# Kernel optimization log

Hardware: AMD Instinct MI355X
Metric: run time of the kernel (lower is better)

The kernel has to match this reference:

```python
import jax, jax.numpy as jnp
import numpy as np

IGNORE_INDEX = -100
LSE_SQUARE_SCALE = 1e-4  # z_loss coefficient


def setup_inputs() -> dict:
    key = jax.random.key(0)
    k1, k2, k3, k4 = jax.random.split(key, 4)
    N, D, V = 4096, 2048, 50257
    inp = {
        "input": jax.random.normal(k1, (N, D), dtype=jnp.float32),
        "weight": jax.random.normal(k2, (V, D), dtype=jnp.float32) * (D ** -0.5),
        "bias": jnp.zeros((V,), dtype=jnp.float32),
        "target": jax.random.randint(k3, (N,), 0, V, dtype=jnp.int64),
    }
    return inp


def reference(input, weight, bias, target):
    # logits: [N, V] = input @ weight.T + bias  (the GEMM the fused kernel chunks)
    logits = jnp.einsum("nd,vd->nv", input, weight) + bias
    lse = jax.nn.logsumexp(logits, axis=-1)  # [N]
    valid = target != IGNORE_INDEX
    safe_tgt = jnp.where(valid, target, 0)
    tgt_logit = jnp.take_along_axis(logits, safe_tgt[:, None], axis=-1)[:, 0]
    ce = lse - tgt_logit                      # per-token cross entropy
    z = LSE_SQUARE_SCALE * lse * lse          # per-token z-loss (lse_square_scale * lse^2)
    per_token = jnp.where(valid, ce + z, 0.0)
    n_valid = jnp.maximum(jnp.sum(valid), 1).astype(per_token.dtype)
    loss = jnp.sum(per_token) / n_valid       # mean over non-ignored tokens (includes z-loss)
    z_loss = jnp.sum(jnp.where(valid, z, 0.0)) / n_valid
    return loss, z_loss
```

## Files before the change

### kernel.cpp

```cpp
#include <hip/hip_runtime.h>
#include <hip/hip_bf16.h>
#include <stdint.h>

#define N_TOK 4096
#define DIM   2048
#define VOCAB 50257
#define VPAD  50304
#define IGNORE_IDX (-100)

typedef short  bf16x8 __attribute__((ext_vector_type(8)));
typedef float  f32x4  __attribute__((ext_vector_type(4)));
typedef unsigned short u16x8 __attribute__((ext_vector_type(8)));

typedef const __attribute__((address_space(1))) unsigned int* gptr_t;
typedef __attribute__((address_space(3))) unsigned int*       lptr_t;

__device__ __forceinline__ unsigned short f2bf(float f) {
  union { float f; uint32_t u; } c; c.f = f;
  uint32_t u = c.u;
  return (unsigned short)((u + 0x7FFFu + ((u >> 16) & 1u)) >> 16);
}

__global__ void cvt_weight(const float* __restrict__ w, unsigned short* __restrict__ o) {
  const int t   = blockIdx.x * 256 + threadIdx.x;
  const int idx = t << 3;
  const int v   = idx >> 11;
  u16x8 r = {0, 0, 0, 0, 0, 0, 0, 0};
  if (v < VOCAB) {
    const float4* p = (const float4*)(w + idx);
    const float4 x0 = p[0];
    const float4 x1 = p[1];
    r[0] = f2bf(x0.x); r[1] = f2bf(x0.y); r[2] = f2bf(x0.z); r[3] = f2bf(x0.w);
    r[4] = f2bf(x1.x); r[5] = f2bf(x1.y); r[6] = f2bf(x1.z); r[7] = f2bf(x1.w);
  }
  *(u16x8*)(o + idx) = r;
}

__global__ void cvt_input(const float* __restrict__ a, unsigned short* __restrict__ o) {
  const int t   = blockIdx.x * 256 + threadIdx.x;
  const int idx = t << 3;
  const float4* p = (const float4*)(a + idx);
  const float4 x0 = p[0];
  const float4 x1 = p[1];
  u16x8 r;
  r[0] = f2bf(x0.x); r[1] = f2bf(x0.y); r[2] = f2bf(x0.z); r[3] = f2bf(x0.w);
  r[4] = f2bf(x1.x); r[5] = f2bf(x1.y); r[6] = f2bf(x1.z); r[7] = f2bf(x1.w);
  *(u16x8*)(o + idx) = r;
}

__global__ __launch_bounds__(256) void flce_gemm(
    const unsigned short* __restrict__ A,
    const unsigned short* __restrict__ B,
    const float* __restrict__ bias,
    const int* __restrict__ target,
    float* __restrict__ sumexp,
    float* __restrict__ tgtlog)
{
  __shared__ unsigned short As[128 * 32];
  __shared__ unsigned short Bs[128 * 32];
  __shared__ int tgt_s[128];

  const int tid  = threadIdx.x;
  const int lane = tid & 63;
  const int wave = tid >> 6;
  const int wm   = wave >> 1;
  const int wn   = wave & 1;
  const int m0   = blockIdx.x * 128;
  const int v0   = blockIdx.y * 128;

  if (tid < 128) tgt_s[tid] = target[m0 + tid];

  const int r0 = tid >> 2;
  const int c0 = (tid & 3) * 8;
  const unsigned short* ag0 = A + (m0 + r0)      * DIM + c0;
  const unsigned short* ag1 = A + (m0 + 64 + r0) * DIM + c0;
  const unsigned short* bg0 = B + (v0 + r0)      * DIM + c0;
  const unsigned short* bg1 = B + (v0 + 64 + r0) * DIM + c0;
  unsigned short* al0 = As + tid * 8;
  unsigned short* al1 = As + (tid + 256) * 8;
  unsigned short* bl0 = Bs + tid * 8;
  unsigned short* bl1 = Bs + (tid + 256) * 8;

  f32x4 acc[4][4];
#pragma unroll
  for (int i = 0; i < 4; i++)
#pragma unroll
    for (int j = 0; j < 4; j++) acc[i][j] = (f32x4){0.f, 0.f, 0.f, 0.f};

  const int mrow = lane & 15;
  const int quad = lane >> 4;

  for (int kt = 0; kt < DIM; kt += 32) {
    __syncthreads();
    __builtin_amdgcn_global_load_lds((gptr_t)(const void*)(ag0 + kt), (lptr_t)(void*)al0, 16, 0, 0);
    __builtin_amdgcn_global_load_lds((gptr_t)(const void*)(ag1 + kt), (lptr_t)(void*)al1, 16, 0, 0);
    __builtin_amdgcn_global_load_lds((gptr_t)(const void*)(bg0 + kt), (lptr_t)(void*)bl0, 16, 0, 0);
    __builtin_amdgcn_global_load_lds((gptr_t)(const void*)(bg1 + kt), (lptr_t)(void*)bl1, 16, 0, 0);
    __syncthreads();

    bf16x8 av[4], bv[4];
#pragma unroll
    for (int f = 0; f < 4; f++)
      av[f] = *(const bf16x8*)(As + (wm * 64 + f * 16 + mrow) * 32 + quad * 8);
#pragma unroll
    for (int f = 0; f < 4; f++)
      bv[f] = *(const bf16x8*)(Bs + (wn * 64 + f * 16 + mrow) * 32 + quad * 8);

#pragma unroll
    for (int i = 0; i < 4; i++)
#pragma unroll
      for (int j = 0; j < 4; j++)
        acc[i][j] = __builtin_amdgcn_mfma_f32_16x16x32_bf16(av[i], bv[j], acc[i][j], 0, 0, 0);
  }

  const int colb = v0 + wn * 64;
#pragma unroll
  for (int i = 0; i < 4; i++) {
    const int rowl = wm * 64 + i * 16 + quad * 4;
    float rs[4] = {0.f, 0.f, 0.f, 0.f};
#pragma unroll
    for (int j = 0; j < 4; j++) {
      const int colg = colb + j * 16 + mrow;
      if (colg < VOCAB) {
        const float bvv = bias[colg];
#pragma unroll
        for (int r = 0; r < 4; r++) {
          const float lg = acc[i][j][r] + bvv;
          rs[r] += __expf(lg);
          if (tgt_s[rowl + r] == colg) tgtlog[m0 + rowl + r] = lg;
        }
      }
    }
#pragma unroll
    for (int r = 0; r < 4; r++) {
      float v = rs[r];
      v += __shfl_xor(v, 1);
      v += __shfl_xor(v, 2);
      v += __shfl_xor(v, 4);
      v += __shfl_xor(v, 8);
      if (mrow == 0) atomicAdd(&sumexp[m0 + rowl + r], v);
    }
  }
}

__global__ void flce_final(const float* __restrict__ sumexp,
                           const float* __restrict__ tgtlog,
                           const int* __restrict__ target,
                           float* __restrict__ out) {
  const int tid = threadIdx.x;
  float ls = 0.f, zs = 0.f;
  int cnt = 0;
  for (int r = tid; r < N_TOK; r += 256) {
    const int t = target[r];
    if (t != IGNORE_IDX) {
      const float lse = logf(sumexp[r]);
      const float z = 1e-4f * lse * lse;
      ls += (lse - tgtlog[r]) + z;
      zs += z;
      cnt++;
    }
  }
#pragma unroll
  for (int off = 32; off > 0; off >>= 1) {
    ls += __shfl_down(ls, off);
    zs += __shfl_down(zs, off);
    cnt += __shfl_down(cnt, off);
  }
  __shared__ float sls[4], szs[4];
  __shared__ int scnt[4];
  const int lane = tid & 63, wv = tid >> 6;
  if (lane == 0) { sls[wv] = ls; szs[wv] = zs; scnt[wv] = cnt; }
  __syncthreads();
  if (tid == 0) {
    float L = 0.f, Z = 0.f;
    int C = 0;
    for (int w = 0; w < 4; w++) { L += sls[w]; Z += szs[w]; C += scnt[w]; }
    const float n = (float)(C > 0 ? C : 1);
    out[0] = L / n;
    out[1] = Z / n;
  }
}

extern "C" void kernel_launch(void* const* d_in, const int* in_sizes, int n_in,
                              void* d_out, int out_size, void* d_ws, size_t ws_size,
                              hipStream_t stream) {
  const float* input  = (const float*)d_in[0];
  const float* weight = (const float*)d_in[1];
  const float* bias   = (const float*)d_in[2];
  const int*   target = (const int*)d_in[3];
  float* out = (float*)d_out;

  unsigned short* wbf = (unsigned short*)d_ws;
  unsigned short* abf = wbf + (size_t)VPAD * DIM;
  float* sumexp = (float*)(abf + (size_t)N_TOK * DIM);
  float* tgtlog = sumexp + N_TOK;

  hipMemsetAsync(sumexp, 0, N_TOK * sizeof(float), stream);
  cvt_weight<<<(VPAD * DIM) / 2048, 256, 0, stream>>>(weight, wbf);
  cvt_input<<<(N_TOK * DIM) / 2048, 256, 0, stream>>>(input, abf);
  flce_gemm<<<dim3(N_TOK / 128, VPAD / 128), 256, 0, stream>>>(abf, wbf, bias, target, sumexp, tgtlog);
  flce_final<<<1, 256, 0, stream>>>(sumexp, tgtlog, target, out);
}
```

Measured before the change: 1.628 ms.

## Double-buffer LDS tiles with XOR swizzle and merge conversion kernels

The GEMM main loop now keeps two LDS buffers and issues the next K-tile's global-to-LDS loads right after a single barrier, instead of loading and computing in strict alternation with two barriers. Both the LDS write positions and the fragment reads use an XOR swizzle on the 16-byte chunk index, meant to reduce LDS bank conflicts. The weight and input fp32-to-bf16 conversion kernels are merged into one launch. The overlap depends on how the compiler places its vmcnt waits for the async LDS loads, and double buffering doubles the LDS use per block.

```diff
diff --git a/kernel.cpp b/kernel.cpp
--- a/kernel.cpp
+++ b/kernel.cpp
@@ -21,31 +21,31 @@
   return (unsigned short)((u + 0x7FFFu + ((u >> 16) & 1u)) >> 16);
 }
 
-__global__ void cvt_weight(const float* __restrict__ w, unsigned short* __restrict__ o) {
-  const int t   = blockIdx.x * 256 + threadIdx.x;
-  const int idx = t << 3;
-  const int v   = idx >> 11;
-  u16x8 r = {0, 0, 0, 0, 0, 0, 0, 0};
-  if (v < VOCAB) {
-    const float4* p = (const float4*)(w + idx);
+__global__ void cvt_all(const float* __restrict__ w, const float* __restrict__ a,
+                        unsigned short* __restrict__ wo, unsigned short* __restrict__ ao) {
+  const long long t   = (long long)blockIdx.x * 256 + threadIdx.x;
+  long long idx = t << 3;
+  if (idx < (long long)VPAD * DIM) {
+    const long long v = idx >> 11;
+    u16x8 r = {0, 0, 0, 0, 0, 0, 0, 0};
+    if (v < VOCAB) {
+      const float4* p = (const float4*)(w + idx);
+      const float4 x0 = p[0];
+      const float4 x1 = p[1];
+      r[0] = f2bf(x0.x); r[1] = f2bf(x0.y); r[2] = f2bf(x0.z); r[3] = f2bf(x0.w);
+      r[4] = f2bf(x1.x); r[5] = f2bf(x1.y); r[6] = f2bf(x1.z); r[7] = f2bf(x1.w);
+    }
+    *(u16x8*)(wo + idx) = r;
+  } else {
+    idx -= (long long)VPAD * DIM;
+    const float4* p = (const float4*)(a + idx);
     const float4 x0 = p[0];
     const float4 x1 = p[1];
+    u16x8 r;
     r[0] = f2bf(x0.x); r[1] = f2bf(x0.y); r[2] = f2bf(x0.z); r[3] = f2bf(x0.w);
     r[4] = f2bf(x1.x); r[5] = f2bf(x1.y); r[6] = f2bf(x1.z); r[7] = f2bf(x1.w);
-  }
-  *(u16x8*)(o + idx) = r;
-}
-
-__global__ void cvt_input(const float* __restrict__ a, unsigned short* __restrict__ o) {
-  const int t   = blockIdx.x * 256 + threadIdx.x;
-  const int idx = t << 3;
-  const float4* p = (const float4*)(a + idx);
-  const float4 x0 = p[0];
-  const float4 x1 = p[1];
-  u16x8 r;
-  r[0] = f2bf(x0.x); r[1] = f2bf(x0.y); r[2] = f2bf(x0.z); r[3] = f2bf(x0.w);
-  r[4] = f2bf(x1.x); r[5] = f2bf(x1.y); r[6] = f2bf(x1.z); r[7] = f2bf(x1.w);
-  *(u16x8*)(o + idx) = r;
+    *(u16x8*)(ao + idx) = r;
+  }
 }
 
 __global__ __launch_bounds__(256) void flce_gemm(
@@ -56,8 +56,8 @@
     float* __restrict__ sumexp,
     float* __restrict__ tgtlog)
 {
-  __shared__ unsigned short As[128 * 32];
-  __shared__ unsigned short Bs[128 * 32];
+  __shared__ unsigned short As[2][128 * 32];
+  __shared__ unsigned short Bs[2][128 * 32];
   __shared__ int tgt_s[128];
 
   const int tid  = threadIdx.x;
@@ -70,16 +70,12 @@
 
   if (tid < 128) tgt_s[tid] = target[m0 + tid];
 
-  const int r0 = tid >> 2;
-  const int c0 = (tid & 3) * 8;
-  const unsigned short* ag0 = A + (m0 + r0)      * DIM + c0;
-  const unsigned short* ag1 = A + (m0 + 64 + r0) * DIM + c0;
-  const unsigned short* bg0 = B + (v0 + r0)      * DIM + c0;
-  const unsigned short* bg1 = B + (v0 + 64 + r0) * DIM + c0;
-  unsigned short* al0 = As + tid * 8;
-  unsigned short* al1 = As + (tid + 256) * 8;
-  unsigned short* bl0 = Bs + tid * 8;
-  unsigned short* bl1 = Bs + (tid + 256) * 8;
+  const int r0  = tid >> 2;
+  const int c0s = ((tid & 3) ^ ((tid >> 3) & 3)) * 8;
+  const unsigned short* ag0 = A + (m0 + r0)      * DIM + c0s;
+  const unsigned short* ag1 = A + (m0 + 64 + r0) * DIM + c0s;
+  const unsigned short* bg0 = B + (v0 + r0)      * DIM + c0s;
+  const unsigned short* bg1 = B + (v0 + 64 + r0) * DIM + c0s;
 
   f32x4 acc[4][4];
 #pragma unroll
@@ -89,22 +85,36 @@
 
   const int mrow = lane & 15;
   const int quad = lane >> 4;
-
-  for (int kt = 0; kt < DIM; kt += 32) {
+  const int swz  = quad ^ ((mrow >> 1) & 3);
+
+#define STAGE(bufi, kt) do {                                                             \
+    unsigned short* a_ = As[bufi]; unsigned short* b_ = Bs[bufi];                        \
+    __builtin_amdgcn_global_load_lds((gptr_t)(const void*)(ag0 + (kt)),                  \
+                                     (lptr_t)(void*)(a_ + tid * 8),         16, 0, 0);   \
+    __builtin_amdgcn_global_load_lds((gptr_t)(const void*)(ag1 + (kt)),                  \
+                                     (lptr_t)(void*)(a_ + (tid + 256) * 8), 16, 0, 0);   \
+    __builtin_amdgcn_global_load_lds((gptr_t)(const void*)(bg0 + (kt)),                  \
+                                     (lptr_t)(void*)(b_ + tid * 8),         16, 0, 0);   \
+    __builtin_amdgcn_global_load_lds((gptr_t)(const void*)(bg1 + (kt)),                  \
+                                     (lptr_t)(void*)(b_ + (tid + 256) * 8), 16, 0, 0);   \
+  } while (0)
+
+  STAGE(0, 0);
+
+  const int NK = DIM / 32;
+  for (int t = 0; t < NK; t++) {
     __syncthreads();
-    __builtin_amdgcn_global_load_lds((gptr_t)(const void*)(ag0 + kt), (lptr_t)(void*)al0, 16, 0, 0);
-    __builtin_amdgcn_global_load_lds((gptr_t)(const void*)(ag1 + kt), (lptr_t)(void*)al1, 16, 0, 0);
-    __builtin_amdgcn_global_load_lds((gptr_t)(const void*)(bg0 + kt), (lptr_t)(void*)bl0, 16, 0, 0);
-    __builtin_amdgcn_global_load_lds((gptr_t)(const void*)(bg1 + kt), (lptr_t)(void*)bl1, 16, 0, 0);
-    __syncthreads();
-
+    if (t + 1 < NK) STAGE((t + 1) & 1, (t + 1) * 32);
+
+    const unsigned short* a_ = As[t & 1];
+    const unsigned short* b_ = Bs[t & 1];
     bf16x8 av[4], bv[4];
 #pragma unroll
     for (int f = 0; f < 4; f++)
-      av[f] = *(const bf16x8*)(As + (wm * 64 + f * 16 + mrow) * 32 + quad * 8);
+      av[f] = *(const bf16x8*)(a_ + ((wm * 64 + f * 16 + mrow) * 4 + swz) * 8);
 #pragma unroll
     for (int f = 0; f < 4; f++)
-      bv[f] = *(const bf16x8*)(Bs + (wn * 64 + f * 16 + mrow) * 32 + quad * 8);
+      bv[f] = *(const bf16x8*)(b_ + ((wn * 64 + f * 16 + mrow) * 4 + swz) * 8);
 
 #pragma unroll
     for (int i = 0; i < 4; i++)
@@ -112,6 +122,7 @@
       for (int j = 0; j < 4; j++)
         acc[i][j] = __builtin_amdgcn_mfma_f32_16x16x32_bf16(av[i], bv[j], acc[i][j], 0, 0, 0);
   }
+#undef STAGE
 
   const int colb = v0 + wn * 64;
 #pragma unroll
@@ -196,8 +207,7 @@
   float* tgtlog = sumexp + N_TOK;
 
   hipMemsetAsync(sumexp, 0, N_TOK * sizeof(float), stream);
-  cvt_weight<<<(VPAD * DIM) / 2048, 256, 0, stream>>>(weight, wbf);
-  cvt_input<<<(N_TOK * DIM) / 2048, 256, 0, stream>>>(input, abf);
+  cvt_all<<<((VPAD + N_TOK) * (long long)DIM) / 2048, 256, 0, stream>>>(weight, input, wbf, abf);
   flce_gemm<<<dim3(N_TOK / 128, VPAD / 128), 256, 0, stream>>>(abf, wbf, bias, target, sumexp, tgtlog);
   flce_final<<<1, 256, 0, stream>>>(sumexp, tgtlog, target, out);
 }
```

After: 2.031 ms. 1.25x slower.
